# Kernel tuning notes

Measured on AMD Instinct MI355X. Metric: run time of the kernel, lower is better.

## Reference

```python
import jax, jax.numpy as jnp
import numpy as np

B, S, D, H, NH, C = 32, 512, 768, 768, 4, 10
HD = H // NH


def _lin(x, w, b):
    return x @ w.T + b


def _ln(x, g, b, eps=1e-5):
    mu = jnp.mean(x, axis=-1, keepdims=True)
    var = jnp.mean(jnp.square(x - mu), axis=-1, keepdims=True)
    return (x - mu) * jax.lax.rsqrt(var + eps) * g + b


def setup_inputs() -> dict:
    key = jax.random.key(0)
    ks = jax.random.split(key, 16)
    w = lambda k, shape: jax.random.normal(k, shape, dtype=jnp.float32) * 0.02
    return {
        "x": jax.random.normal(ks[0], (B, S, D), dtype=jnp.float32),
        "wq": w(ks[1], (H, D)), "bq": jnp.zeros((H,), jnp.float32),
        "wk": w(ks[2], (H, D)), "bk": jnp.zeros((H,), jnp.float32),
        "wv": w(ks[3], (H, D)), "bv": jnp.zeros((H,), jnp.float32),
        "wx": w(ks[4], (H, D)), "bx": jnp.zeros((H,), jnp.float32),
        "in_proj_w": w(ks[5], (3 * H, H)), "in_proj_b": jnp.zeros((3 * H,), jnp.float32),
        "out_proj_w": w(ks[6], (H, H)), "out_proj_b": jnp.zeros((H,), jnp.float32),
        "fc1a_w": w(ks[7], (H, H)), "fc1a_b": jnp.zeros((H,), jnp.float32),
        "fc1b_w": w(ks[8], (H, H)), "fc1b_b": jnp.zeros((H,), jnp.float32),
        "ln_g": jnp.ones((H,), jnp.float32), "ln_b": jnp.zeros((H,), jnp.float32),
        "fc2_w": w(ks[9], (C, H)), "fc2_b": jnp.zeros((C,), jnp.float32),
    }


def reference(x, wq, bq, wk, bk, wv, bv, wx, bx, in_proj_w, in_proj_b,
              out_proj_w, out_proj_b, fc1a_w, fc1a_b, fc1b_w, fc1b_b,
              ln_g, ln_b, fc2_w, fc2_b):
    # Vectorized sinusoidal PE matching the triple loop:
    # even i: sin(pos / 10000^(2i/D)); odd i: cos(pos / 10000^(2(i-1)/D))
    d = x.shape[2]
    pos = jnp.arange(x.shape[1], dtype=x.dtype)[:, None]          # [S,1]
    i = jnp.arange(d)
    i_even = (i - (i % 2)).astype(x.dtype)                        # 2*(i - i%2)/d exponent
    angle = pos / jnp.power(jnp.asarray(10000.0, x.dtype), 2.0 * i_even / d)  # [S,D]
    pe = jnp.where(i % 2 == 0, jnp.sin(angle), jnp.cos(angle))
    x = x + pe[None]

    q = _lin(x, wq, bq)
    k = _lin(x, wk, bk)
    v = _lin(x, wv, bv)
    xr = _lin(x, wx, bx)

    # torch MultiheadAttention: in_proj, split heads, SDPA, out_proj
    wq_i, wk_i, wv_i = jnp.split(in_proj_w, 3, axis=0)
    bq_i, bk_i, bv_i = jnp.split(in_proj_b, 3, axis=0)
    b = x.shape[0]
    q2 = _lin(q, wq_i, bq_i).reshape(b, -1, NH, HD)
    k2 = _lin(k, wk_i, bk_i).reshape(b, -1, NH, HD)
    v2 = _lin(v, wv_i, bv_i).reshape(b, -1, NH, HD)
    scores = jnp.einsum('bqhd,bkhd->bhqk', q2, k2) / jnp.sqrt(jnp.asarray(HD, x.dtype))
    attn = jax.nn.softmax(scores, axis=-1)
    ctx = jnp.einsum('bhqk,bkhd->bqhd', attn, v2).reshape(b, -1, H)
    attn_out = _lin(ctx, out_proj_w, out_proj_b)

    x = _ln(xr + attn_out, ln_g, ln_b)
    ffn = _lin(jax.nn.relu(_lin(x, fc1a_w, fc1a_b)), fc1b_w, fc1b_b)
    x = _ln(x + ffn, ln_g, ln_b)
    x = jnp.sum(x, axis=1)
    return _lin(x, fc2_w, fc2_b)
```

## Files before the change

### kernel.cpp

```cpp
#include <hip/hip_runtime.h>
#include <hip/hip_bf16.h>

typedef __bf16 bf16;
typedef __bf16 bf16x8 __attribute__((ext_vector_type(8)));
typedef __bf16 bf16x4 __attribute__((ext_vector_type(4)));
typedef __bf16 bf16x2 __attribute__((ext_vector_type(2)));
typedef float  f32x4  __attribute__((ext_vector_type(4)));

#define GLD16(g, l) __builtin_amdgcn_global_load_lds(                        \
    (const __attribute__((address_space(1))) void*)(g),                      \
    (__attribute__((address_space(3))) void*)(l), 16, 0, 0)

template<int BM, int BN, int MFR, int NFR>
__global__ __launch_bounds__(256, 3)
void gemm_nt(const bf16* __restrict__ A, const bf16* __restrict__ B,
             bf16* __restrict__ C, const float* __restrict__ bias,
             int K, int lda, int ldb, int ldc,
             int inner,
             long long aOut, long long aIn,
             long long bOut, long long bIn,
             long long cOut, long long cIn,
             float alpha, int relu,
             const bf16* __restrict__ res, int ldr)
{
    const int z  = blockIdx.z;
    const int zo = z / inner;
    const int zi = z - zo * inner;
    A += (long long)zo * aOut + (long long)zi * aIn;
    B += (long long)zo * bOut + (long long)zi * bIn;
    C += (long long)zo * cOut + (long long)zi * cIn;

    const int tm = blockIdx.y * BM;
    const int tn = blockIdx.x * BN;

    __shared__ __align__(16) bf16 smem[(BM + BN) * 64];
    bf16* As = smem;
    bf16* Bs = smem + BM * 64;

    const int tid  = threadIdx.x;
    const int lane = tid & 63;
    const int wid  = tid >> 6;
    const int wr   = wid >> 1;
    const int wc   = wid & 1;

    f32x4 acc[MFR][NFR];
#pragma unroll
    for (int i = 0; i < MFR; ++i)
#pragma unroll
        for (int j = 0; j < NFR; ++j) acc[i][j] = (f32x4){0.f, 0.f, 0.f, 0.f};

    const int srow = lane >> 3;
    const int gch8 = ((lane & 7) ^ srow) * 8;

    const int NA = BM / 32;
    const int NB = BN / 32;

    const bf16* aP[NA];
#pragma unroll
    for (int jj = 0; jj < NA; ++jj) {
        const int R0 = (wid * NA + jj) * 8;
        aP[jj] = A + (long long)(tm + R0 + srow) * lda + gch8;
    }
    const bf16* bP[NB];
#pragma unroll
    for (int jj = 0; jj < NB; ++jj) {
        const int R0 = (wid * NB + jj) * 8;
        bP[jj] = B + (long long)(tn + R0 + srow) * ldb + gch8;
    }

    const int lr = lane & 15;
    const int qg = lane >> 4;

    for (int kt = 0; kt < K; kt += 64) {
#pragma unroll
        for (int jj = 0; jj < NA; ++jj)
            GLD16(aP[jj], As + (wid * NA + jj) * 512);
#pragma unroll
        for (int jj = 0; jj < NB; ++jj)
            GLD16(bP[jj], Bs + (wid * NB + jj) * 512);
        __syncthreads();

#pragma unroll
        for (int h = 0; h < 2; ++h) {
            const int off = ((qg + h * 4) ^ (lr & 7)) * 8;
            bf16x8 af[MFR], bfr[NFR];
#pragma unroll
            for (int i = 0; i < MFR; ++i)
                af[i] = *(const bf16x8*)(As + (wr * MFR * 16 + i * 16 + lr) * 64 + off);
#pragma unroll
            for (int j = 0; j < NFR; ++j)
                bfr[j] = *(const bf16x8*)(Bs + (wc * NFR * 16 + j * 16 + lr) * 64 + off);
#pragma unroll
            for (int i = 0; i < MFR; ++i)
#pragma unroll
                for (int j = 0; j < NFR; ++j)
                    acc[i][j] = __builtin_amdgcn_mfma_f32_16x16x32_bf16(
                        af[i], bfr[j], acc[i][j], 0, 0, 0);
        }
        __syncthreads();
#pragma unroll
        for (int jj = 0; jj < NA; ++jj) aP[jj] += 64;
#pragma unroll
        for (int jj = 0; jj < NB; ++jj) bP[jj] += 64;
    }

#pragma unroll
    for (int i = 0; i < MFR; ++i) {
#pragma unroll
        for (int j = 0; j < NFR; ++j) {
            const int mm0 = tm + wr * MFR * 16 + i * 16 + (lane >> 4) * 4;
            const int nn  = tn + wc * NFR * 16 + j * 16 + (lane & 15);
#pragma unroll
            for (int r = 0; r < 4; ++r) {
                float v = acc[i][j][r] * alpha;
                if (bias) v += bias[nn];
                if (res)  v += (float)res[(long long)(mm0 + r) * ldr + nn];
                if (relu) v = fmaxf(v, 0.f);
                C[(long long)(mm0 + r) * ldc + nn] = (bf16)v;
            }
        }
    }
}

__global__ __launch_bounds__(256, 2)
void fused_attn_kernel(bf16* __restrict__ qkvx)
{
    const int flat = blockIdx.x;
    const int qt = (flat >> 3) & 3;
    const int z  = (flat & 7) | ((flat >> 5) << 3);
    const int b  = z >> 2, h = z & 3;

    const bf16* Qg = qkvx + (long long)b * 512 * 3072 + h * 192;
    const bf16* Kg = Qg + 768;
    const bf16* Vg = Qg + 1536;

    __shared__ __align__(16) bf16 Ks[64 * 192];
    __shared__ __align__(16) bf16 VTs[192 * 64];
    __shared__ __align__(16) bf16 Pb[4 * 32 * 64];

    const int tid  = threadIdx.x;
    const int lane = tid & 63;
    const int wid  = tid >> 6;
    const int lr   = lane & 15;
    const int qg   = lane >> 4;
    const int m0   = qt * 128 + wid * 32;

    bf16x8 qf[2][6];
#pragma unroll
    for (int mt = 0; mt < 2; ++mt)
#pragma unroll
        for (int t = 0; t < 6; ++t)
            qf[mt][t] = *(const bf16x8*)(Qg + (long long)(m0 + mt * 16 + lr) * 3072
                                         + t * 32 + qg * 8);

    const bf16* kP[6];
#pragma unroll
    for (int i = 0; i < 6; ++i) {
        const int c = i * 256 + tid;
        const int krow = c / 24, kcc = c % 24;
        const int kgc  = (kcc & 24) | ((kcc & 7) ^ (krow & 7));
        kP[i] = Kg + (long long)krow * 3072 + kgc * 8;
    }
    const int vkp = tid & 31;
    const int vdc = tid >> 5;

    f32x4 acc[2][12];
#pragma unroll
    for (int mt = 0; mt < 2; ++mt)
#pragma unroll
        for (int dt = 0; dt < 12; ++dt) acc[mt][dt] = (f32x4){0.f, 0.f, 0.f, 0.f};
    float mrow[2][4], lrow[2][4];
#pragma unroll
    for (int mt = 0; mt < 2; ++mt)
#pragma unroll
        for (int r = 0; r < 4; ++r) { mrow[mt][r] = -3e38f; lrow[mt][r] = 0.f; }

    const float alpha = 0.0721687836f;

    for (int kt = 0; kt < 8; ++kt) {
#pragma unroll
        for (int i = 0; i < 6; ++i)
            GLD16(kP[i], Ks + (i * 256 + wid * 64) * 8);
#pragma unroll
        for (int i = 0; i < 3; ++i) {
            const int dc = vdc + i * 8;
            const bf16* p = Vg + (long long)(2 * vkp) * 3072 + dc * 8;
            const bf16x8 v0 = *(const bf16x8*)(p);
            const bf16x8 v1 = *(const bf16x8*)(p + 3072);
#pragma unroll
            for (int j = 0; j < 8; ++j) {
                const int d = dc * 8 + j;
                bf16x2 pk; pk[0] = v0[j]; pk[1] = v1[j];
                *(bf16x2*)(VTs + d * 64 + ((vkp >> 2) ^ (d & 7)) * 8
                           + 2 * (vkp & 3)) = pk;
            }
        }
        __syncthreads();

        f32x4 sf[2][4];
#pragma unroll
        for (int mt = 0; mt < 2; ++mt)
#pragma unroll
            for (int nt = 0; nt < 4; ++nt) sf[mt][nt] = (f32x4){0.f, 0.f, 0.f, 0.f};
#pragma unroll
        for (int nt = 0; nt < 4; ++nt) {
#pragma unroll
            for (int t = 0; t < 6; ++t) {
                const int ch = t * 4 + qg;
                const int ph = (ch & 24) | ((ch & 7) ^ (lr & 7));
                const bf16x8 kf = *(const bf16x8*)(Ks + (nt * 16 + lr) * 192 + ph * 8);
                sf[0][nt] = __builtin_amdgcn_mfma_f32_16x16x32_bf16(qf[0][t], kf, sf[0][nt], 0, 0, 0);
                sf[1][nt] = __builtin_amdgcn_mfma_f32_16x16x32_bf16(qf[1][t], kf, sf[1][nt], 0, 0, 0);
            }
        }

#pragma unroll
        for (int mt = 0; mt < 2; ++mt) {
            float mx[4], a[4], rs[4], p[4][4];
#pragma unroll
            for (int r = 0; r < 4; ++r) {
                float v0 = fmaxf(sf[mt][0][r], sf[mt][1][r]);
                float v1 = fmaxf(sf[mt][2][r], sf[mt][3][r]);
                mx[r] = fmaxf(v0, v1) * alpha;
            }
#pragma unroll
            for (int msk = 1; msk <= 8; msk <<= 1)
#pragma unroll
                for (int r = 0; r < 4; ++r) mx[r] = fmaxf(mx[r], __shfl_xor(mx[r], msk));
#pragma unroll
            for (int r = 0; r < 4; ++r) {
                const float mn = fmaxf(mrow[mt][r], mx[r]);
                a[r] = __expf(mrow[mt][r] - mn);
                mrow[mt][r] = mn;
                rs[r] = 0.f;
            }
#pragma unroll
            for (int nt = 0; nt < 4; ++nt)
#pragma unroll
                for (int r = 0; r < 4; ++r) {
                    p[nt][r] = __expf(sf[mt][nt][r] * alpha - mrow[mt][r]);
                    rs[r] += p[nt][r];
                }
#pragma unroll
            for (int msk = 1; msk <= 8; msk <<= 1)
#pragma unroll
                for (int r = 0; r < 4; ++r) rs[r] += __shfl_xor(rs[r], msk);
#pragma unroll
            for (int r = 0; r < 4; ++r) lrow[mt][r] = lrow[mt][r] * a[r] + rs[r];
#pragma unroll
            for (int dt = 0; dt < 12; ++dt)
#pragma unroll
                for (int r = 0; r < 4; ++r) acc[mt][dt][r] *= a[r];
#pragma unroll
            for (int nt = 0; nt < 4; ++nt)
#pragma unroll
                for (int r = 0; r < 4; ++r) {
                    const int row = mt * 16 + qg * 4 + r;
                    const int ph2 = (nt * 2 + (lr >> 3)) ^ (row & 7);
                    Pb[wid * 2048 + row * 64 + ph2 * 8 + (lr & 7)] = (bf16)p[nt][r];
                }
        }

        bf16x8 pf[2][2];
#pragma unroll
        for (int mt = 0; mt < 2; ++mt)
#pragma unroll
            for (int ks = 0; ks < 2; ++ks) {
                const int row = mt * 16 + lr;
                const int ph  = (ks * 4 + qg) ^ (lr & 7);
                pf[mt][ks] = *(const bf16x8*)(Pb + wid * 2048 + row * 64 + ph * 8);
            }
#pragma unroll
        for (int dt = 0; dt < 12; ++dt) {
#pragma unroll
            for (int ks = 0; ks < 2; ++ks) {
                const int ph = (ks * 4 + qg) ^ (lr & 7);
                const bf16x8 vf = *(const bf16x8*)(VTs + (dt * 16 + lr) * 64 + ph * 8);
                acc[0][dt] = __builtin_amdgcn_mfma_f32_16x16x32_bf16(pf[0][ks], vf, acc[0][dt], 0, 0, 0);
                acc[1][dt] = __builtin_amdgcn_mfma_f32_16x16x32_bf16(pf[1][ks], vf, acc[1][dt], 0, 0, 0);
            }
        }
        __syncthreads();
#pragma unroll
        for (int i = 0; i < 6; ++i) kP[i] += 64 * 3072;
        Vg += 64 * 3072;
    }

    bf16* Og = qkvx + (long long)b * 512 * 3072 + h * 192;
#pragma unroll
    for (int mt = 0; mt < 2; ++mt) {
        float inv[4];
#pragma unroll
        for (int r = 0; r < 4; ++r) inv[r] = 1.0f / lrow[mt][r];
#pragma unroll
        for (int dt = 0; dt < 12; ++dt)
#pragma unroll
            for (int r = 0; r < 4; ++r) {
                const int row = m0 + mt * 16 + qg * 4 + r;
                Og[(long long)row * 3072 + dt * 16 + lr] = (bf16)(acc[mt][dt][r] * inv[r]);
            }
    }
}

__device__ __forceinline__ void cast4(const float* src, bf16* dst, int i)
{
    const float4 v = *(const float4*)(src + (long long)i * 4);
    bf16x4 o;
    o[0] = (bf16)v.x; o[1] = (bf16)v.y; o[2] = (bf16)v.z; o[3] = (bf16)v.w;
    *(bf16x4*)(dst + (long long)i * 4) = o;
}

__global__ __launch_bounds__(256)
void prep_kernel(const float* __restrict__ wq, const float* __restrict__ wk,
                 const float* __restrict__ wv, const float* __restrict__ wx,
                 const float* __restrict__ inpw, const float* __restrict__ inpb,
                 const float* __restrict__ bq, const float* __restrict__ bk,
                 const float* __restrict__ bv, const float* __restrict__ bx,
                 const float* __restrict__ woutp, const float* __restrict__ wf1a,
                 const float* __restrict__ wf1b, const float* __restrict__ x,
                 bf16* __restrict__ WT3, bf16* __restrict__ INPJ,
                 bf16* __restrict__ WOUT, bf16* __restrict__ WF1A,
                 bf16* __restrict__ WF1B, bf16* __restrict__ WXD,
                 float* __restrict__ BCAT, bf16* __restrict__ XPE)
{
    const int blk = blockIdx.x;
    const int tid = threadIdx.x;
    __shared__ bf16 t[32][33];

    if (blk < 1728) {
        const int which = blk / 576, local = blk - which * 576;
        const float* src = (which == 0) ? wq : ((which == 1) ? wk : wv);
        bf16* dst = WT3 + (long long)which * 589824;
        const int r0 = (local / 24) * 32, c0 = (local % 24) * 32;
        const int tr = tid >> 5, tc = tid & 31;
#pragma unroll
        for (int k = 0; k < 4; ++k) {
            const int r = tr + k * 8;
            t[r][tc] = (bf16)src[(long long)(r0 + r) * 768 + c0 + tc];
        }
        __syncthreads();
#pragma unroll
        for (int k = 0; k < 4; ++k) {
            const int c = tr + k * 8;
            dst[(long long)(c0 + c) * 768 + r0 + tc] = t[tc][c];
        }
    } else if (blk < 3456) {
        cast4(inpw, INPJ, (blk - 1728) * 256 + tid);
    } else if (blk < 4032) {
        cast4(woutp, WOUT, (blk - 3456) * 256 + tid);
    } else if (blk < 4608) {
        cast4(wf1a, WF1A, (blk - 4032) * 256 + tid);
    } else if (blk < 5184) {
        cast4(wf1b, WF1B, (blk - 4608) * 256 + tid);
    } else if (blk < 5760) {
        cast4(wx, WXD, (blk - 5184) * 256 + tid);
    } else if (blk < 6051) {
        const int bl = blk - 5760;
        if (bl < 288) {
            const int g = tid >> 5, l = tid & 31;
            const int n = bl * 8 + g;
            const int zsec = n / 768;
            const float* bb = (zsec == 0) ? bq : ((zsec == 1) ? bk : bv);
            const float* wrow = inpw + (long long)n * 768;
            float s = 0.f;
            for (int d = l; d < 768; d += 32) s += wrow[d] * bb[d];
#pragma unroll
            for (int off = 16; off; off >>= 1) s += __shfl_xor(s, off);
            if (l == 0) BCAT[n] = inpb[n] + s;
        } else {
            const int n = (bl - 288) * 256 + tid;
            if (n < 768) BCAT[2304 + n] = bx[n];
        }
    } else {
        const int idx4 = ((blk - 6051) * 256 + tid) * 4;
        const int d    = idx4 % 768;
        const int row  = idx4 / 768;
        const int s    = row & 511;
        const float ksc = -0.034603417655076f;
        const float4 xv = *(const float4*)(x + (long long)idx4);
        float a0 = (float)s * exp2f((float)d * ksc);
        float a1 = (float)s * exp2f((float)(d + 2) * ksc);
        float s0, c0, s1, c1;
        sincosf(a0, &s0, &c0);
        sincosf(a1, &s1, &c1);
        bf16x4 o;
        o[0] = (bf16)(xv.x + s0);
        o[1] = (bf16)(xv.y + c0);
        o[2] = (bf16)(xv.z + s1);
        o[3] = (bf16)(xv.w + c1);
        *(bf16x4*)(XPE + (long long)idx4) = o;
    }
}

__global__ __launch_bounds__(192)
void ln1_kernel(const bf16* __restrict__ a, int lda_,
                bf16* __restrict__ o, int ldo,
                const float* __restrict__ g, const float* __restrict__ be)
{
    const int row = blockIdx.x;
    const int t   = threadIdx.x;
    const int d0  = t * 4;
    const bf16x4 av = *(const bf16x4*)(a + (long long)row * lda_ + d0);
    float xv[4];
#pragma unroll
    for (int k = 0; k < 4; ++k) xv[k] = (float)av[k];
    float s1 = xv[0] + xv[1] + xv[2] + xv[3];
    float s2 = xv[0]*xv[0] + xv[1]*xv[1] + xv[2]*xv[2] + xv[3]*xv[3];
    for (int off = 32; off; off >>= 1) {
        s1 += __shfl_xor(s1, off);
        s2 += __shfl_xor(s2, off);
    }
    __shared__ float red[6];
    const int wid = t >> 6, lane = t & 63;
    if (lane == 0) { red[wid] = s1; red[3 + wid] = s2; }
    __syncthreads();
    s1 = red[0] + red[1] + red[2];
    s2 = red[3] + red[4] + red[5];
    const float mu  = s1 * (1.0f / 768.0f);
    const float var = s2 * (1.0f / 768.0f) - mu * mu;
    const float rs  = rsqrtf(var + 1e-5f);
    const float4 gv = *(const float4*)(g + d0);
    const float4 ev = *(const float4*)(be + d0);
    bf16x4 ov;
    ov[0] = (bf16)(((xv[0] - mu) * rs) * gv.x + ev.x);
    ov[1] = (bf16)(((xv[1] - mu) * rs) * gv.y + ev.y);
    ov[2] = (bf16)(((xv[2] - mu) * rs) * gv.z + ev.z);
    ov[3] = (bf16)(((xv[3] - mu) * rs) * gv.w + ev.w);
    *(bf16x4*)(o + (long long)row * ldo + d0) = ov;
}

__global__ __launch_bounds__(256)
void ln2_reduce_kernel(const bf16* __restrict__ src,
                       const float* __restrict__ g, const float* __restrict__ be,
                       float* __restrict__ partial)
{
    const int blk  = blockIdx.x;
    const int tid  = threadIdx.x;
    const int wid  = tid >> 6, lane = tid & 63;
    const int d0   = lane * 12;

    float gv[12], ev[12];
#pragma unroll
    for (int k = 0; k < 12; k += 4) {
        *(float4*)(gv + k) = *(const float4*)(g + d0 + k);
        *(float4*)(ev + k) = *(const float4*)(be + d0 + k);
    }
    float acc[12];
#pragma unroll
    for (int k = 0; k < 12; ++k) acc[k] = 0.f;

    for (int i = 0; i < 8; ++i) {
        const int row = blk * 32 + i * 4 + wid;
        const bf16* p = src + (long long)row * 3072 + d0;
        float xv[12];
#pragma unroll
        for (int k = 0; k < 12; k += 4) {
            const bf16x4 v = *(const bf16x4*)(p + k);
            xv[k] = (float)v[0]; xv[k+1] = (float)v[1];
            xv[k+2] = (float)v[2]; xv[k+3] = (float)v[3];
        }
        float s1 = 0.f, s2 = 0.f;
#pragma unroll
        for (int k = 0; k < 12; ++k) { s1 += xv[k]; s2 += xv[k] * xv[k]; }
        for (int off = 32; off; off >>= 1) {
            s1 += __shfl_xor(s1, off);
            s2 += __shfl_xor(s2, off);
        }
        const float mu  = s1 * (1.0f / 768.0f);
        const float var = s2 * (1.0f / 768.0f) - mu * mu;
        const float rs  = rsqrtf(var + 1e-5f);
#pragma unroll
        for (int k = 0; k < 12; ++k) acc[k] += (xv[k] - mu) * rs * gv[k] + ev[k];
    }

    __shared__ float red[4][768];
#pragma unroll
    for (int k = 0; k < 12; k += 4)
        *(float4*)(&red[wid][d0 + k]) = *(const float4*)(acc + k);
    __syncthreads();
    if (wid == 0) {
#pragma unroll
        for (int k = 0; k < 12; k += 4) {
            const float4 a0 = *(const float4*)(&red[0][d0 + k]);
            const float4 a1 = *(const float4*)(&red[1][d0 + k]);
            const float4 a2 = *(const float4*)(&red[2][d0 + k]);
            const float4 a3 = *(const float4*)(&red[3][d0 + k]);
            *(float4*)(partial + (long long)blk * 768 + d0 + k) =
                make_float4(a0.x + a1.x + a2.x + a3.x, a0.y + a1.y + a2.y + a3.y,
                            a0.z + a1.z + a2.z + a3.z, a0.w + a1.w + a2.w + a3.w);
        }
    }
}

__global__ __launch_bounds__(192)
void reduce_fc2_stage2_kernel(const float* __restrict__ partial, const float* __restrict__ w,
                              const float* __restrict__ bias, float* __restrict__ out)
{
    const int b = blockIdx.x, t = threadIdx.x;
    const int d0 = t * 4;
    float a[4] = {0.f, 0.f, 0.f, 0.f};
    for (int c = 0; c < 16; ++c) {
        const float4 pv = *(const float4*)(partial + (long long)(b * 16 + c) * 768 + d0);
        a[0] += pv.x; a[1] += pv.y; a[2] += pv.z; a[3] += pv.w;
    }
    __shared__ float os[10];
    if (t < 10) os[t] = 0.f;
    __syncthreads();
    for (int c = 0; c < 10; ++c) {
        const float4 wv = *(const float4*)(w + c * 768 + d0);
        float p = wv.x * a[0] + wv.y * a[1] + wv.z * a[2] + wv.w * a[3];
        for (int off = 32; off; off >>= 1) p += __shfl_xor(p, off);
        if ((t & 63) == 0) atomicAdd(&os[c], p);
    }
    __syncthreads();
    if (t < 10) out[b * 10 + t] = os[t] + bias[t];
}

static const size_t OFF_XPE  = 0;
static const size_t OFF_WCAT = OFF_XPE  + (size_t)16384 * 768 * 2;
static const size_t OFF_WT3  = OFF_WCAT + (size_t)3072 * 768 * 2;
static const size_t OFF_INPJ = OFF_WT3  + (size_t)3 * 768 * 768 * 2;
static const size_t OFF_WOUT = OFF_INPJ + (size_t)2304 * 768 * 2;
static const size_t OFF_WF1A = OFF_WOUT + (size_t)768 * 768 * 2;
static const size_t OFF_WF1B = OFF_WF1A + (size_t)768 * 768 * 2;
static const size_t OFF_BCAT = OFF_WF1B + (size_t)768 * 768 * 2;
static const size_t OFF_QKVX = OFF_BCAT + (size_t)3072 * 4;
static const size_t OFF_VT   = OFF_QKVX + (size_t)16384 * 3072 * 2;
static const size_t OFF_S    = OFF_VT   + (size_t)128 * 192 * 512 * 2;
static const size_t OFF_X1   = OFF_S    + (size_t)128 * 512 * 512 * 2;

extern "C" void kernel_launch(void* const* d_in, const int* in_sizes, int n_in,
                              void* d_out, int out_size, void* d_ws, size_t ws_size,
                              hipStream_t stream)
{
    const float* x     = (const float*)d_in[0];
    const float* wq    = (const float*)d_in[1];
    const float* bq    = (const float*)d_in[2];
    const float* wk    = (const float*)d_in[3];
    const float* bk    = (const float*)d_in[4];
    const float* wv    = (const float*)d_in[5];
    const float* bv    = (const float*)d_in[6];
    const float* wx    = (const float*)d_in[7];
    const float* bx    = (const float*)d_in[8];
    const float* inpw  = (const float*)d_in[9];
    const float* inpb  = (const float*)d_in[10];
    const float* woutp = (const float*)d_in[11];
    const float* boutp = (const float*)d_in[12];
    const float* wf1a  = (const float*)d_in[13];
    const float* bf1a  = (const float*)d_in[14];
    const float* wf1b  = (const float*)d_in[15];
    const float* bf1b  = (const float*)d_in[16];
    const float* lng   = (const float*)d_in[17];
    const float* lnb   = (const float*)d_in[18];
    const float* wfc2  = (const float*)d_in[19];
    const float* bfc2  = (const float*)d_in[20];
    float* out = (float*)d_out;

    char* ws = (char*)d_ws;
    bf16*  XPE  = (bf16*)(ws + OFF_XPE);
    bf16*  WCAT = (bf16*)(ws + OFF_WCAT);
    bf16*  WT3  = (bf16*)(ws + OFF_WT3);
    bf16*  INPJ = (bf16*)(ws + OFF_INPJ);
    bf16*  WOUT = (bf16*)(ws + OFF_WOUT);
    bf16*  WF1A = (bf16*)(ws + OFF_WF1A);
    bf16*  WF1B = (bf16*)(ws + OFF_WF1B);
    float* BCAT = (float*)(ws + OFF_BCAT);
    bf16*  QKVX = (bf16*)(ws + OFF_QKVX);
    float* PART = (float*)(ws + OFF_S);
    bf16*  X1   = (bf16*)(ws + OFF_X1);

    prep_kernel<<<18339, 256, 0, stream>>>(wq, wk, wv, wx, inpw, inpb,
                                           bq, bk, bv, bx, woutp, wf1a, wf1b, x,
                                           WT3, INPJ, WOUT, WF1A, WF1B,
                                           WCAT + (size_t)2304 * 768, BCAT, XPE);

    gemm_nt<64, 128, 2, 4><<<dim3(6, 12, 3), 256, 0, stream>>>(
        INPJ, WT3, WCAT, nullptr, 768, 768, 768, 768,
        1, 589824, 0, 589824, 0, 589824, 0, 1.0f, 0, nullptr, 0);

    gemm_nt<128, 128, 4, 4><<<dim3(24, 128, 1), 256, 0, stream>>>(
        XPE, WCAT, QKVX, BCAT, 768, 768, 768, 3072,
        1, 0, 0, 0, 0, 0, 0, 1.0f, 0, nullptr, 0);

    fused_attn_kernel<<<512, 256, 0, stream>>>(QKVX);

    gemm_nt<64, 128, 2, 4><<<dim3(6, 256, 1), 256, 0, stream>>>(
        QKVX, WOUT, QKVX + 768, boutp, 768, 3072, 768, 3072,
        1, 0, 0, 0, 0, 0, 0, 1.0f, 0, QKVX + 2304, 3072);

    ln1_kernel<<<16384, 192, 0, stream>>>(QKVX + 768, 3072, X1, 768, lng, lnb);

    gemm_nt<64, 128, 2, 4><<<dim3(6, 256, 1), 256, 0, stream>>>(
        X1, WF1A, QKVX + 1536, bf1a, 768, 768, 768, 3072,
        1, 0, 0, 0, 0, 0, 0, 1.0f, 1, nullptr, 0);

    gemm_nt<64, 128, 2, 4><<<dim3(6, 256, 1), 256, 0, stream>>>(
        QKVX + 1536, WF1B, QKVX + 2304, bf1b, 768, 3072, 768, 3072,
        1, 0, 0, 0, 0, 0, 0, 1.0f, 0, X1, 768);

    ln2_reduce_kernel<<<512, 256, 0, stream>>>(QKVX + 2304, lng, lnb, PART);

    reduce_fc2_stage2_kernel<<<32, 192, 0, stream>>>(PART, wfc2, bfc2, out);
}
```

Before: 507.5 us.

## Add specialized 256x256 eight-wave QKV GEMM with phased LDS pipeline

Replaces the generic 128x128 GEMM for the large fused QKVX projection with a dedicated 512-thread kernel using 256x256 tiles, double-buffered swizzled LDS staging via global_load_lds, and an interleaved phase schedule of LDS reads, MFMAs and barriers with priority boosts. The goal is higher MFMA utilization and more data reuse per tile on the dominant GEMM. It hard-codes K=768 and the output stride, and the larger tile produces fewer blocks (768), with heavy register and LDS use per block.

```diff
diff --git a/kernel.cpp b/kernel.cpp
--- a/kernel.cpp
+++ b/kernel.cpp
@@ -118,6 +118,136 @@
                 if (relu) v = fmaxf(v, 0.f);
                 C[(long long)(mm0 + r) * ldc + nn] = (bf16)v;
             }
+        }
+    }
+}
+
+#define BAR8()  __builtin_amdgcn_s_barrier()
+#define LGKM0() do { asm volatile("s_waitcnt lgkmcnt(0)" ::: "memory");      \
+                     __builtin_amdgcn_sched_barrier(0); } while (0)
+
+#define RD_A(S, MB)                                                          \
+    _Pragma("unroll") for (int mi = 0; mi < 4; ++mi)                         \
+    _Pragma("unroll") for (int h = 0; h < 2; ++h)                            \
+        af[mi][h] = *(const bf16x8*)((S) + aBase + ((MB) + mi) * 1024 +      \
+                                     (h ? koff1 : koff0));
+
+#define RD_B(S, NJ)                                                          \
+    _Pragma("unroll") for (int h = 0; h < 2; ++h)                            \
+        bfv[NJ][h] = *(const bf16x8*)((S) + bBase + (NJ) * 1024 +            \
+                                      (h ? koff1 : koff0));
+
+#define MFMA_Q(MB, N0, N1)                                                   \
+    __builtin_amdgcn_s_setprio(1);                                          \
+    _Pragma("unroll") for (int h = 0; h < 2; ++h)                            \
+    _Pragma("unroll") for (int mi = 0; mi < 4; ++mi) {                       \
+        acc[(MB)+mi][(N0)] = __builtin_amdgcn_mfma_f32_16x16x32_bf16(        \
+            af[mi][h], bfv[(N0)][h], acc[(MB)+mi][(N0)], 0, 0, 0);           \
+        acc[(MB)+mi][(N1)] = __builtin_amdgcn_mfma_f32_16x16x32_bf16(        \
+            af[mi][h], bfv[(N1)][h], acc[(MB)+mi][(N1)], 0, 0, 0);           \
+    }                                                                        \
+    __builtin_amdgcn_s_setprio(0);
+
+#define STAGE8(DST)                                                          \
+    _Pragma("unroll") for (int jj = 0; jj < 4; ++jj)                         \
+        GLD16(aP[jj], (DST) + (wid * 4 + jj) * 512);                         \
+    _Pragma("unroll") for (int jj = 0; jj < 4; ++jj)                         \
+        GLD16(bP[jj], (DST) + 16384 + (wid * 4 + jj) * 512);                 \
+    _Pragma("unroll") for (int jj = 0; jj < 4; ++jj) { aP[jj] += 64; bP[jj] += 64; }
+
+#define K_TILE(S, DO_STAGE, SYNC)                                            \
+  {                                                                          \
+    RD_A((S), 0); RD_B((S), 0); RD_B((S), 1);                                \
+    BAR8(); LGKM0();                                                         \
+    MFMA_Q(0, 0, 1)                                                          \
+    BAR8();                                                                  \
+    RD_B((S), 2); RD_B((S), 3);                                              \
+    BAR8(); LGKM0();                                                         \
+    MFMA_Q(0, 2, 3)                                                          \
+    BAR8();                                                                  \
+    RD_A((S), 4);                                                            \
+    BAR8(); LGKM0();                                                         \
+    MFMA_Q(4, 2, 3)                                                          \
+    BAR8();                                                                  \
+    if (DO_STAGE) { STAGE8((S)) }                                            \
+    BAR8();                                                                  \
+    MFMA_Q(4, 0, 1)                                                          \
+    if ((SYNC) == 0) asm volatile("s_waitcnt vmcnt(8)" ::: "memory");        \
+    if ((SYNC) == 1) asm volatile("s_waitcnt vmcnt(0)" ::: "memory");        \
+    if ((SYNC) != 2) BAR8();                                                 \
+  }
+
+__global__ __launch_bounds__(512, 2)
+void gemm_qkv_8ph(const bf16* __restrict__ A, const bf16* __restrict__ B,
+                  bf16* __restrict__ C, const float* __restrict__ bias)
+{
+    constexpr int LDA = 768, LDB = 768, LDC = 3072;
+    const int tm = blockIdx.y * 256;
+    const int tn = blockIdx.x * 256;
+
+    __shared__ __align__(16) bf16 smem[2][2 * 256 * 64];
+
+    const int tid  = threadIdx.x;
+    const int lane = tid & 63;
+    const int wid  = tid >> 6;
+    const int wr   = wid >> 2;
+    const int wc   = wid & 3;
+    const int lr   = lane & 15;
+    const int qg   = lane >> 4;
+
+    const int srow = lane >> 3;
+    const int gch8 = ((lane & 7) ^ srow) * 8;
+    const bf16* aP[4];
+    const bf16* bP[4];
+#pragma unroll
+    for (int jj = 0; jj < 4; ++jj) {
+        aP[jj] = A + (long long)(tm + wid * 32 + jj * 8 + srow) * LDA + gch8;
+        bP[jj] = B + (long long)(tn + wid * 32 + jj * 8 + srow) * LDB + gch8;
+    }
+
+    f32x4 acc[8][4];
+#pragma unroll
+    for (int i = 0; i < 8; ++i)
+#pragma unroll
+        for (int j = 0; j < 4; ++j) acc[i][j] = (f32x4){0.f, 0.f, 0.f, 0.f};
+
+    const int aBase = (wr * 128 + lr) * 64;
+    const int bBase = 16384 + (wc * 64 + lr) * 64;
+    const int koff0 = ((qg    ) ^ (lr & 7)) * 8;
+    const int koff1 = ((qg + 4) ^ (lr & 7)) * 8;
+
+    bf16x8 af[4][2];
+    bf16x8 bfv[4][2];
+
+    bf16* S0 = &smem[0][0];
+    bf16* S1 = &smem[1][0];
+
+    STAGE8(S0)
+    STAGE8(S1)
+    asm volatile("s_waitcnt vmcnt(8)" ::: "memory");
+    BAR8();
+
+#pragma unroll 1
+    for (int it = 0; it < 5; ++it) {
+        K_TILE(S0, 1, 0)
+        K_TILE(S1, 1, 0)
+    }
+    K_TILE(S0, 0, 1)
+    K_TILE(S1, 0, 2)
+
+    float bv[4];
+#pragma unroll
+    for (int j = 0; j < 4; ++j) bv[j] = bias[tn + wc * 64 + j * 16 + lr];
+
+#pragma unroll
+    for (int i = 0; i < 8; ++i) {
+        const int mm0 = tm + wr * 128 + i * 16 + qg * 4;
+#pragma unroll
+        for (int j = 0; j < 4; ++j) {
+            const int nn = tn + wc * 64 + j * 16 + lr;
+#pragma unroll
+            for (int r = 0; r < 4; ++r)
+                C[(long long)(mm0 + r) * LDC + nn] = (bf16)(acc[i][j][r] + bv[j]);
         }
     }
 }
@@ -578,9 +708,7 @@
         INPJ, WT3, WCAT, nullptr, 768, 768, 768, 768,
         1, 589824, 0, 589824, 0, 589824, 0, 1.0f, 0, nullptr, 0);
 
-    gemm_nt<128, 128, 4, 4><<<dim3(24, 128, 1), 256, 0, stream>>>(
-        XPE, WCAT, QKVX, BCAT, 768, 768, 768, 3072,
-        1, 0, 0, 0, 0, 0, 0, 1.0f, 0, nullptr, 0);
+    gemm_qkv_8ph<<<dim3(12, 64, 1), 512, 0, stream>>>(XPE, WCAT, QKVX, BCAT);
 
     fused_attn_kernel<<<512, 256, 0, stream>>>(QKVX);
 
```

New measurement: 491.6 us. 1.03x faster.
